# Kernel optimization log

Hardware: AMD Instinct MI355X
Metric: run time of the kernel (lower is better)

Reference implementation:

```python
import jax, jax.numpy as jnp
import numpy as np


def setup_inputs() -> dict:
    key = jax.random.key(0)
    k1, k2 = jax.random.split(key)
    z = jax.random.normal(k1, (16, 256, 32, 32), dtype=jnp.float32)
    emb = jax.random.normal(k2, (8192, 256), dtype=jnp.float32)
    return {"z": z, "emb": emb}


def reference(z, emb):
    B, C, H, W = z.shape
    # [B,C,H,W] -> [B*H*W, C], distances in fp32 for precision
    z_f = jnp.transpose(z, (0, 2, 3, 1)).reshape(-1, C).astype(jnp.float32)
    e = emb.astype(jnp.float32)
    # squared-distance expansion: ||z||^2 - 2 z.e + ||e||^2  -> [N, K]
    d = (
        jnp.sum(z_f * z_f, axis=1, keepdims=True)
        - 2.0 * (z_f @ e.T)
        + jnp.sum(e * e, axis=1)[None, :]
    )
    idx = jnp.argmin(d, axis=1)  # [N]
    out = emb[idx].astype(z.dtype)  # codebook gather
    return jnp.transpose(out.reshape(B, H, W, C), (0, 3, 1, 2))
```

## Files before the change

### kernel.cpp

```cpp
#include <hip/hip_runtime.h>
#include <stdint.h>

#define NB   16
#define CD   256
#define HW   1024
#define NQ   16384
#define KCN  8192

typedef unsigned long long u64;
typedef unsigned short     u16;
using f32x4  = __attribute__((ext_vector_type(4))) float;
using bf16x8 = __attribute__((ext_vector_type(8))) __bf16;

#define ZTB_OFF  0
#define EMBB_OFF 8388608
#define EH_OFF   12582912
#define CAND_OFF 12615680

static __device__ __forceinline__ void gl_lds16(const void* g, void* l) {
  __builtin_amdgcn_global_load_lds(
      (const __attribute__((address_space(1))) void*)g,
      (__attribute__((address_space(3))) void*)l, 16, 0, 0);
}

static __device__ __forceinline__ unsigned bf16r(float x) {
  unsigned u = __float_as_uint(x);
  return (u + 0x7fffu + ((u >> 16) & 1u)) >> 16;
}

static __device__ __forceinline__ u64 umin64(u64 a, u64 b) { return a < b ? a : b; }
static __device__ __forceinline__ u64 umax64(u64 a, u64 b) { return a < b ? b : a; }

__global__ __launch_bounds__(256) void k_prep(const float* __restrict__ z,
                                              const float* __restrict__ emb,
                                              u16* __restrict__ zTb,
                                              u16* __restrict__ embB,
                                              float* __restrict__ eH) {
  const int bx = (int)blockIdx.x;
  if (bx < 1024) {
    __shared__ float tile[64][65];
    const int b   = bx >> 6;
    const int hwT = (bx >> 2) & 15;
    const int cT  = bx & 3;
    const int tx  = threadIdx.x & 63;
    const int ty  = threadIdx.x >> 6;
    const float* src = z + (size_t)(b * CD + cT * 64) * HW + hwT * 64;
#pragma unroll
    for (int i = 0; i < 16; ++i) {
      const int c_l = ty + 4 * i;
      tile[c_l][tx] = src[(size_t)c_l * HW + tx];
    }
    __syncthreads();
    const size_t dbase = (size_t)(b * HW + hwT * 64) * CD + cT * 64;
#pragma unroll
    for (int i = 0; i < 16; ++i) {
      const int hw_l = ty + 4 * i;
      zTb[dbase + (size_t)hw_l * CD + tx] = (u16)bf16r(tile[tx][hw_l]);
    }
  } else {
    const int wave = (bx - 1024) * 4 + ((int)threadIdx.x >> 6);
    const int lane = threadIdx.x & 63;
#pragma unroll
    for (int it = 0; it < 8; ++it) {
      const int row = wave * 8 + it;
      const float4 v = *(const float4*)(emb + (size_t)row * CD + lane * 4);
      uint2 pk;
      pk.x = bf16r(v.x) | (bf16r(v.y) << 16);
      pk.y = bf16r(v.z) | (bf16r(v.w) << 16);
      *(uint2*)(embB + (size_t)row * CD + lane * 4) = pk;
      float s = v.x * v.x + v.y * v.y + v.z * v.z + v.w * v.w;
#pragma unroll
      for (int off = 32; off; off >>= 1) s += __shfl_xor(s, off, 64);
      if (lane == 0) eH[row] = 0.5f * s + 1024.0f;
    }
  }
}


#define WAITV(N) asm volatile("s_waitcnt vmcnt(" #N ")" ::: "memory")
#define MEMFENCE() asm volatile("" ::: "memory")

__global__ __launch_bounds__(256, 2) void k_argmin(const u16* __restrict__ zTb,
                                                   const u16* __restrict__ embB,
                                                   const float* __restrict__ eH,
                                                   u64* __restrict__ cand) {
  __shared__ __align__(16) u16 Bs[4][64 * 128];

  const int tid  = (int)threadIdx.x;
  const int w    = tid >> 6;
  const int lane = tid & 63;
  const int l15  = lane & 15, quad = lane >> 4;
  const int q0    = (int)(blockIdx.x >> 3) * 128;
  const int split = (int)(blockIdx.x & 7);
  const int wq0 = (w & 1) * 64;
  const int nh  = w >> 1;

  bf16x8 Af[4][2][4];
  {
    const char* aB = (const char*)zTb + (size_t)(q0 + wq0 + l15) * 512 + quad * 16;
#pragma unroll
    for (int i = 0; i < 4; ++i)
#pragma unroll
      for (int kc = 0; kc < 2; ++kc)
#pragma unroll
        for (int ks = 0; ks < 4; ++ks)
          Af[i][kc][ks] = *(const bf16x8*)(aB + i * 8192 + kc * 256 + ks * 64);
  }
  MEMFENCE();

  const char* bS = (const char*)embB + (size_t)split * 524288
                 + (size_t)(tid >> 4) * 512
                 + (size_t)(((tid & 15) ^ ((tid >> 4) & 7)) * 16);
  const int ldsW = tid * 16;

#define STAGE(RING, SRCOFF)                                                    \
  do {                                                                         \
    const char* _s = bP + (SRCOFF);                                            \
    char* _d = (char*)Bs[RING] + ldsW;                                         \
    gl_lds16(_s,         _d);                                                  \
    gl_lds16(_s + 8192,  _d + 4096);                                           \
    gl_lds16(_s + 16384, _d + 8192);                                           \
    gl_lds16(_s + 24576, _d + 12288);                                          \
    MEMFENCE();                                                                \
  } while (0)

  const int bRow = (nh * 32 + l15) * 256;
  const int gx   = l15 & 7;

#define MFMA_INT(RING, KCH)                                                    \
  do {                                                                         \
    const char* _b = (const char*)Bs[RING] + bRow;                             \
    __builtin_amdgcn_s_setprio(1);                                             \
    _Pragma("unroll")                                                          \
    for (int ks = 0; ks < 4; ++ks) {                                           \
      const int _o = ((ks * 4 + quad) ^ gx) * 16;                              \
      const bf16x8 bf0 = *(const bf16x8*)(_b + _o);                            \
      const bf16x8 bf1 = *(const bf16x8*)(_b + 4096 + _o);                     \
      _Pragma("unroll")                                                        \
      for (int i = 0; i < 4; ++i)                                              \
        acc[i][0] = __builtin_amdgcn_mfma_f32_16x16x32_bf16(Af[i][KCH][ks],    \
                                                            bf0, acc[i][0],    \
                                                            0, 0, 0);          \
      _Pragma("unroll")                                                        \
      for (int i = 0; i < 4; ++i)                                              \
        acc[i][1] = __builtin_amdgcn_mfma_f32_16x16x32_bf16(Af[i][KCH][ks],    \
                                                            bf1, acc[i][1],    \
                                                            0, 0, 0);          \
    }                                                                          \
    __builtin_amdgcn_s_setprio(0);                                             \
  } while (0)

#define ACCZERO()                                                              \
  do {                                                                         \
    _Pragma("unroll")                                                          \
    for (int i = 0; i < 4; ++i) {                                              \
      acc[i][0] = f32x4{0.f, 0.f, 0.f, 0.f};                                   \
      acc[i][1] = f32x4{0.f, 0.f, 0.f, 0.f};                                   \
    }                                                                          \
  } while (0)

#define EPILOGUE(NC, EH0, EH1)                                                 \
  do {                                                                         \
    _Pragma("unroll")                                                          \
    for (int i = 0; i < 4; ++i)                                                \
      _Pragma("unroll")                                                        \
      for (int r = 0; r < 4; ++r) {                                            \
        const int s = i * 4 + r;                                               \
        const unsigned kb0 = (__float_as_uint((EH0) - acc[i][0][r]) & ~31u)    \
                             | (unsigned)((NC) * 2 + 0);                       \
        const unsigned kb1 = (__float_as_uint((EH1) - acc[i][1][r]) & ~31u)    \
                             | (unsigned)((NC) * 2 + 1);                       \
        const float k0 = __uint_as_float(kb0), k1 = __uint_as_float(kb1);      \
        const float lo = fminf(k0, k1), hi = fmaxf(k0, k1);                    \
        b2[s] = fminf(fmaxf(lo, b1[s]), fminf(hi, b2[s]));                     \
        b1[s] = fminf(lo, b1[s]);                                              \
      }                                                                        \
  } while (0)

  f32x4 acc[4][2];
  float b1[16], b2[16];
  const float FMAX = __uint_as_float(0x7F7FFFFFu);
#pragma unroll
  for (int s = 0; s < 16; ++s) { b1[s] = FMAX; b2[s] = FMAX; }

  const float* ehP = eH + split * 1024 + nh * 32 + l15;
  float ehA[2], ehB[2], ehAn[2], ehBn[2];

  const char* bP = bS;
  STAGE(0, 0);
  ehA[0] = ehP[0];  ehA[1] = ehP[16];  MEMFENCE();
  STAGE(1, 256);
  STAGE(2, 32768);
  ehB[0] = ehP[64]; ehB[1] = ehP[80]; MEMFENCE();
  const float* ehPn = ehP + 128;

  for (int ntp = 0; ntp < 7; ++ntp) {
    const int nca = 2 * ntp, ncb = 2 * ntp + 1;

    ACCZERO();
    WAITV(12); __builtin_amdgcn_s_barrier(); MEMFENCE();
    STAGE(3, 33024);
    MFMA_INT(0, 0);

    WAITV(10); __builtin_amdgcn_s_barrier(); MEMFENCE();
    STAGE(0, 65536);
    ehAn[0] = ehPn[0]; ehAn[1] = ehPn[16]; MEMFENCE();
    MFMA_INT(1, 1);
    EPILOGUE(nca, ehA[0], ehA[1]);

    ACCZERO();
    WAITV(12); __builtin_amdgcn_s_barrier(); MEMFENCE();
    STAGE(1, 65792);
    MFMA_INT(2, 0);

    WAITV(10); __builtin_amdgcn_s_barrier(); MEMFENCE();
    STAGE(2, 98304);
    ehBn[0] = ehPn[64]; ehBn[1] = ehPn[80]; MEMFENCE();
    MFMA_INT(3, 1);
    EPILOGUE(ncb, ehB[0], ehB[1]);

    ehA[0] = ehAn[0]; ehA[1] = ehAn[1];
    ehB[0] = ehBn[0]; ehB[1] = ehBn[1];
    bP += 65536;
    ehPn += 128;
  }

  {
    ACCZERO();
    WAITV(12); __builtin_amdgcn_s_barrier(); MEMFENCE();
    STAGE(3, 33024);
    MFMA_INT(0, 0);

    WAITV(10); __builtin_amdgcn_s_barrier(); MEMFENCE();
    MFMA_INT(1, 1);
    EPILOGUE(14, ehA[0], ehA[1]);

    ACCZERO();
    WAITV(6); __builtin_amdgcn_s_barrier(); MEMFENCE();
    MFMA_INT(2, 0);

    WAITV(0); __builtin_amdgcn_s_barrier(); MEMFENCE();
    MFMA_INT(3, 1);
    EPILOGUE(15, ehB[0], ehB[1]);
  }
#undef STAGE
#undef MFMA_INT
#undef ACCZERO
#undef EPILOGUE

#pragma unroll
  for (int s = 0; s < 16; ++s) {
    u64 x1 = ((u64)__float_as_uint(b1[s]) << 32) | (unsigned)l15;
    u64 x2 = ((u64)__float_as_uint(b2[s]) << 32) | (unsigned)l15;
#pragma unroll
    for (int off = 1; off < 16; off <<= 1) {
      const u64 o1 = __shfl_xor(x1, off, 64);
      const u64 o2 = __shfl_xor(x2, off, 64);
      const u64 lo = umin64(x1, o1);
      const u64 hi = umax64(x1, o1);
      x1 = lo;
      x2 = umin64(hi, umin64(x2, o2));
    }
    if (l15 == 0) {
      const int i = s >> 2, r = s & 3;
      const int q = q0 + wq0 + i * 16 + quad * 4 + r;
      const unsigned kb1 = (unsigned)(x1 >> 32), kb2 = (unsigned)(x2 >> 32);
      const int id1 = (int)(kb1 & 31u), id2 = (int)(kb2 & 31u);
      const int n1 = split * 1024 + (id1 >> 1) * 64 + nh * 32
                     + (id1 & 1) * 16 + (int)(x1 & 15);
      const int n2 = split * 1024 + (id2 >> 1) * 64 + nh * 32
                     + (id2 & 1) * 16 + (int)(x2 & 15);
      cand[(size_t)q * 32 + split * 4 + nh * 2 + 0] = ((u64)kb1 << 32) | (unsigned)n1;
      cand[(size_t)q * 32 + split * 4 + nh * 2 + 1] = ((u64)kb2 << 32) | (unsigned)n2;
    }
  }
}

__global__ __launch_bounds__(256) void k_pick_out(const float* __restrict__ z,
                                                  const float* __restrict__ emb,
                                                  const u64* __restrict__ cand,
                                                  float* __restrict__ out) {
  __shared__ float zs[16][257];
  __shared__ float tile[16][257];
  const int t    = (int)threadIdx.x;
  const int lane = t & 63;
  const int wv   = t >> 6;
  const int sub  = lane >> 4;
  const int l15  = lane & 15;
  const int q0b  = (int)blockIdx.x * 16;
  const int b    = q0b >> 10, hw0 = q0b & 1023;
  const int q    = q0b + wv * 4 + sub;
  const int hwl  = wv * 4 + sub;

  {
    const float* zp = z + ((size_t)(b * CD + t)) * HW + hw0;
    const float4 a0 = *(const float4*)(zp + 0);
    const float4 a1 = *(const float4*)(zp + 4);
    const float4 a2 = *(const float4*)(zp + 8);
    const float4 a3 = *(const float4*)(zp + 12);
    zs[0][t] = a0.x;  zs[1][t] = a0.y;  zs[2][t] = a0.z;  zs[3][t] = a0.w;
    zs[4][t] = a1.x;  zs[5][t] = a1.y;  zs[6][t] = a1.z;  zs[7][t] = a1.w;
    zs[8][t] = a2.x;  zs[9][t] = a2.y;  zs[10][t] = a2.z; zs[11][t] = a2.w;
    zs[12][t] = a3.x; zs[13][t] = a3.y; zs[14][t] = a3.z; zs[15][t] = a3.w;
  }
  __syncthreads();

  const u64* cp = cand + (size_t)q * 32 + l15 * 2;
  const u64 v0 = cp[0], v1 = cp[1];
  u64 s0 = umin64(v0, v1), s1 = umax64(v0, v1), s2 = ~0ull, s3 = ~0ull;
#pragma unroll
  for (int off = 1; off < 16; off <<= 1) {
    const u64 b0 = __shfl_xor(s0, off, 64);
    const u64 b1 = __shfl_xor(s1, off, 64);
    const u64 b2 = __shfl_xor(s2, off, 64);
    const u64 b3 = __shfl_xor(s3, off, 64);
    const u64 c0 = umin64(s0, b0);
    const u64 c1 = umin64(umin64(s1, b1), umax64(s0, b0));
    const u64 c2 = umin64(umin64(s2, b2),
                          umin64(umax64(s1, b0), umax64(s0, b1)));
    const u64 c3 = umin64(umin64(umin64(s3, b3), umax64(s2, b0)),
                          umin64(umax64(s0, b2), umax64(s1, b1)));
    s0 = c0; s1 = c1; s2 = c2; s3 = c3;
  }
  const u64 sel[4] = {s0, s1, s2, s3};

  float zq[16];
#pragma unroll
  for (int j = 0; j < 16; ++j) zq[j] = zs[hwl][j * 16 + l15];

  double bd = 1e300;
  int bi = 0x7fffffff;
  float keep[16];
#pragma unroll
  for (int j = 0; j < 16; ++j) keep[j] = 0.f;
#pragma unroll
  for (int c4 = 0; c4 < 4; ++c4) {
    const int idx = (int)(unsigned)(sel[c4] & 0xffffffffull);
    const float* er = emb + (size_t)idx * CD;
    float ev[16];
#pragma unroll
    for (int j = 0; j < 16; ++j) ev[j] = er[j * 16 + l15];
    double s = 0.0;
#pragma unroll
    for (int j = 0; j < 16; ++j) {
      const double d = (double)zq[j] - (double)ev[j];
      s += d * d;
    }
#pragma unroll
    for (int off = 1; off < 16; off <<= 1) s += __shfl_xor(s, off, 64);
    const bool better = (s < bd) || (s == bd && idx < bi);
    if (better) {
      bd = s; bi = idx;
#pragma unroll
      for (int j = 0; j < 16; ++j) keep[j] = ev[j];
    }
  }
#pragma unroll
  for (int j = 0; j < 16; ++j) tile[hwl][j * 16 + l15] = keep[j];
  __syncthreads();
  const int cluster = t >> 4;
  const int ll      = t & 15;
  float* obase = out + (size_t)b * CD * HW + hw0 + ll;
#pragma unroll
  for (int j = 0; j < 16; ++j) {
    const int c = 16 * j + cluster;
    obase[(size_t)c * HW] = tile[ll][c];
  }
}

extern "C" void kernel_launch(void* const* d_in, const int* in_sizes, int n_in,
                              void* d_out, int out_size, void* d_ws, size_t ws_size,
                              hipStream_t stream) {
  const float* z   = (const float*)d_in[0];
  const float* emb = (const float*)d_in[1];
  float* out = (float*)d_out;

  char* ws = (char*)d_ws;
  u16*   zTb  = (u16*)(ws + ZTB_OFF);
  u16*   embB = (u16*)(ws + EMBB_OFF);
  float* eH   = (float*)(ws + EH_OFF);
  u64*   cand = (u64*)(ws + CAND_OFF);

  k_prep<<<1280, 256, 0, stream>>>(z, emb, zTb, embB, eH);
  k_argmin<<<1024, 256, 0, stream>>>(zTb, embB, eH, cand);
  k_pick_out<<<1024, 256, 0, stream>>>(z, emb, cand, out);
}
```

Before: 176.7 us.

## Give each wave a private LDS double buffer and drop block barriers

The 4-slot shared ring that all four waves filled cooperatively is replaced by a private two-slot LDS buffer per wave. Each wave stages only the codebook rows it consumes, so the s_barrier calls can go and waits use only vmcnt/lgkmcnt. All B fragments for a K-chunk are read from LDS up front, and the next chunk's global-to-LDS copy is issued into the same slot right after those reads. This removes block-wide synchronisation stalls between waves. The cost is that waves sharing the same rows now load them separately, so global traffic rises, and each wave has fewer tiles in flight.

```diff
diff --git a/kernel.cpp b/kernel.cpp
--- a/kernel.cpp
+++ b/kernel.cpp
@@ -78,13 +78,14 @@
 
 
 #define WAITV(N) asm volatile("s_waitcnt vmcnt(" #N ")" ::: "memory")
+#define LGKM0()  asm volatile("s_waitcnt lgkmcnt(0)" ::: "memory")
 #define MEMFENCE() asm volatile("" ::: "memory")
 
 __global__ __launch_bounds__(256, 2) void k_argmin(const u16* __restrict__ zTb,
                                                    const u16* __restrict__ embB,
                                                    const float* __restrict__ eH,
                                                    u64* __restrict__ cand) {
-  __shared__ __align__(16) u16 Bs[4][64 * 128];
+  __shared__ __align__(16) u16 Bs[4][2][4096];
 
   const int tid  = (int)threadIdx.x;
   const int w    = tid >> 6;
@@ -108,58 +109,94 @@
   }
   MEMFENCE();
 
-  const char* bS = (const char*)embB + (size_t)split * 524288
-                 + (size_t)(tid >> 4) * 512
-                 + (size_t)(((tid & 15) ^ ((tid >> 4) & 7)) * 16);
-  const int ldsW = tid * 16;
-
-#define STAGE(RING, SRCOFF)                                                    \
+  char* myLds0 = (char*)&Bs[w][0][0];
+  char* myLds1 = myLds0 + 8192;
+  const int lane16 = lane * 16;
+
+  const char* bW = (const char*)embB
+                 + (size_t)(split * 1024 + nh * 32 + (lane >> 3)) * 512
+                 + (size_t)(((lane & 7) ^ (lane >> 3)) * 16);
+
+#define STAGE(SLOT, SRC)                                                       \
   do {                                                                         \
-    const char* _s = bP + (SRCOFF);                                            \
-    char* _d = (char*)Bs[RING] + ldsW;                                         \
-    gl_lds16(_s,         _d);                                                  \
-    gl_lds16(_s + 8192,  _d + 4096);                                           \
-    gl_lds16(_s + 16384, _d + 8192);                                           \
-    gl_lds16(_s + 24576, _d + 12288);                                          \
+    const char* _s = (SRC);                                                    \
+    char* _d = (SLOT) + lane16;                                                \
+    gl_lds16(_s,          _d);                                                 \
+    gl_lds16(_s + 4096,   _d + 1024);                                          \
+    gl_lds16(_s + 8192,   _d + 2048);                                          \
+    gl_lds16(_s + 12288,  _d + 3072);                                          \
+    gl_lds16(_s + 128,    _d + 4096);                                          \
+    gl_lds16(_s + 4224,   _d + 5120);                                          \
+    gl_lds16(_s + 8320,   _d + 6144);                                          \
+    gl_lds16(_s + 12416,  _d + 7168);                                          \
     MEMFENCE();                                                                \
   } while (0)
 
-  const int bRow = (nh * 32 + l15) * 256;
-  const int gx   = l15 & 7;
-
-#define MFMA_INT(RING, KCH)                                                    \
+  const int gx = l15 & 7;
+  const int oA = (quad ^ gx) * 16;
+  const int oB = ((4 + quad) ^ gx) * 16;
+
+  f32x4 acc[4][2];
+  float b1[16], b2[16];
+  const float FMAX = __uint_as_float(0x7F7FFFFFu);
+#pragma unroll
+  for (int s = 0; s < 16; ++s) { b1[s] = FMAX; b2[s] = FMAX; }
+
+#define ACCZERO()                                                              \
   do {                                                                         \
-    const char* _b = (const char*)Bs[RING] + bRow;                             \
+    _Pragma("unroll")                                                          \
+    for (int i = 0; i < 4; ++i) {                                              \
+      acc[i][0] = f32x4{0.f, 0.f, 0.f, 0.f};                                   \
+      acc[i][1] = f32x4{0.f, 0.f, 0.f, 0.f};                                   \
+    }                                                                          \
+  } while (0)
+
+#define COMPUTE(SB, KC, ...)                                                   \
+  do {                                                                         \
+    const char* _sb = (const char*)(SB) + l15 * 128;                           \
+    bf16x8 f00 = *(const bf16x8*)(_sb + oA);                                   \
+    bf16x8 f01 = *(const bf16x8*)(_sb + 2048 + oA);                            \
+    bf16x8 f10 = *(const bf16x8*)(_sb + oB);                                   \
+    bf16x8 f11 = *(const bf16x8*)(_sb + 2048 + oB);                            \
+    bf16x8 f20 = *(const bf16x8*)(_sb + 4096 + oA);                            \
+    bf16x8 f21 = *(const bf16x8*)(_sb + 6144 + oA);                            \
+    bf16x8 f30 = *(const bf16x8*)(_sb + 4096 + oB);                            \
+    bf16x8 f31 = *(const bf16x8*)(_sb + 6144 + oB);                            \
+    LGKM0();                                                                   \
+    __VA_ARGS__;                                                               \
     __builtin_amdgcn_s_setprio(1);                                             \
     _Pragma("unroll")                                                          \
-    for (int ks = 0; ks < 4; ++ks) {                                           \
-      const int _o = ((ks * 4 + quad) ^ gx) * 16;                              \
-      const bf16x8 bf0 = *(const bf16x8*)(_b + _o);                            \
-      const bf16x8 bf1 = *(const bf16x8*)(_b + 4096 + _o);                     \
-      _Pragma("unroll")                                                        \
-      for (int i = 0; i < 4; ++i)                                              \
-        acc[i][0] = __builtin_amdgcn_mfma_f32_16x16x32_bf16(Af[i][KCH][ks],    \
-                                                            bf0, acc[i][0],    \
-                                                            0, 0, 0);          \
-      _Pragma("unroll")                                                        \
-      for (int i = 0; i < 4; ++i)                                              \
-        acc[i][1] = __builtin_amdgcn_mfma_f32_16x16x32_bf16(Af[i][KCH][ks],    \
-                                                            bf1, acc[i][1],    \
-                                                            0, 0, 0);          \
+    for (int i = 0; i < 4; ++i) {                                              \
+      acc[i][0] = __builtin_amdgcn_mfma_f32_16x16x32_bf16(Af[i][KC][0], f00,   \
+                                                          acc[i][0], 0, 0, 0); \
+      acc[i][1] = __builtin_amdgcn_mfma_f32_16x16x32_bf16(Af[i][KC][0], f01,   \
+                                                          acc[i][1], 0, 0, 0); \
+    }                                                                          \
+    _Pragma("unroll")                                                          \
+    for (int i = 0; i < 4; ++i) {                                              \
+      acc[i][0] = __builtin_amdgcn_mfma_f32_16x16x32_bf16(Af[i][KC][1], f10,   \
+                                                          acc[i][0], 0, 0, 0); \
+      acc[i][1] = __builtin_amdgcn_mfma_f32_16x16x32_bf16(Af[i][KC][1], f11,   \
+                                                          acc[i][1], 0, 0, 0); \
+    }                                                                          \
+    _Pragma("unroll")                                                          \
+    for (int i = 0; i < 4; ++i) {                                              \
+      acc[i][0] = __builtin_amdgcn_mfma_f32_16x16x32_bf16(Af[i][KC][2], f20,   \
+                                                          acc[i][0], 0, 0, 0); \
+      acc[i][1] = __builtin_amdgcn_mfma_f32_16x16x32_bf16(Af[i][KC][2], f21,   \
+                                                          acc[i][1], 0, 0, 0); \
+    }                                                                          \
+    _Pragma("unroll")                                                          \
+    for (int i = 0; i < 4; ++i) {                                              \
+      acc[i][0] = __builtin_amdgcn_mfma_f32_16x16x32_bf16(Af[i][KC][3], f30,   \
+                                                          acc[i][0], 0, 0, 0); \
+      acc[i][1] = __builtin_amdgcn_mfma_f32_16x16x32_bf16(Af[i][KC][3], f31,   \
+                                                          acc[i][1], 0, 0, 0); \
     }                                                                          \
     __builtin_amdgcn_s_setprio(0);                                             \
   } while (0)
 
-#define ACCZERO()                                                              \
-  do {                                                                         \
-    _Pragma("unroll")                                                          \
-    for (int i = 0; i < 4; ++i) {                                              \
-      acc[i][0] = f32x4{0.f, 0.f, 0.f, 0.f};                                   \
-      acc[i][1] = f32x4{0.f, 0.f, 0.f, 0.f};                                   \
-    }                                                                          \
-  } while (0)
-
-#define EPILOGUE(NC, EH0, EH1)                                                 \
+#define EPILOGUE(NT, EH0, EH1)                                                 \
   do {                                                                         \
     _Pragma("unroll")                                                          \
     for (int i = 0; i < 4; ++i)                                                \
@@ -167,9 +204,9 @@
       for (int r = 0; r < 4; ++r) {                                            \
         const int s = i * 4 + r;                                               \
         const unsigned kb0 = (__float_as_uint((EH0) - acc[i][0][r]) & ~31u)    \
-                             | (unsigned)((NC) * 2 + 0);                       \
+                             | (unsigned)((NT) * 2 + 0);                       \
         const unsigned kb1 = (__float_as_uint((EH1) - acc[i][1][r]) & ~31u)    \
-                             | (unsigned)((NC) * 2 + 1);                       \
+                             | (unsigned)((NT) * 2 + 1);                       \
         const float k0 = __uint_as_float(kb0), k1 = __uint_as_float(kb1);      \
         const float lo = fminf(k0, k1), hi = fmaxf(k0, k1);                    \
         b2[s] = fminf(fmaxf(lo, b1[s]), fminf(hi, b2[s]));                     \
@@ -177,74 +214,39 @@
       }                                                                        \
   } while (0)
 
-  f32x4 acc[4][2];
-  float b1[16], b2[16];
-  const float FMAX = __uint_as_float(0x7F7FFFFFu);
-#pragma unroll
-  for (int s = 0; s < 16; ++s) { b1[s] = FMAX; b2[s] = FMAX; }
-
   const float* ehP = eH + split * 1024 + nh * 32 + l15;
-  float ehA[2], ehB[2], ehAn[2], ehBn[2];
-
-  const char* bP = bS;
-  STAGE(0, 0);
-  ehA[0] = ehP[0];  ehA[1] = ehP[16];  MEMFENCE();
-  STAGE(1, 256);
-  STAGE(2, 32768);
-  ehB[0] = ehP[64]; ehB[1] = ehP[80]; MEMFENCE();
-  const float* ehPn = ehP + 128;
-
-  for (int ntp = 0; ntp < 7; ++ntp) {
-    const int nca = 2 * ntp, ncb = 2 * ntp + 1;
-
+  float ehA0, ehA1, ehN0 = 0.f, ehN1 = 0.f;
+
+  const char* bC = bW;
+  STAGE(myLds0, bC);
+  ehA0 = ehP[0]; ehA1 = ehP[16]; MEMFENCE();
+  STAGE(myLds1, bC + 256);
+  const float* ehN = ehP + 64;
+
+  for (int nt = 0; nt < 15; ++nt) {
     ACCZERO();
-    WAITV(12); __builtin_amdgcn_s_barrier(); MEMFENCE();
-    STAGE(3, 33024);
-    MFMA_INT(0, 0);
-
-    WAITV(10); __builtin_amdgcn_s_barrier(); MEMFENCE();
-    STAGE(0, 65536);
-    ehAn[0] = ehPn[0]; ehAn[1] = ehPn[16]; MEMFENCE();
-    MFMA_INT(1, 1);
-    EPILOGUE(nca, ehA[0], ehA[1]);
-
-    ACCZERO();
-    WAITV(12); __builtin_amdgcn_s_barrier(); MEMFENCE();
-    STAGE(1, 65792);
-    MFMA_INT(2, 0);
-
-    WAITV(10); __builtin_amdgcn_s_barrier(); MEMFENCE();
-    STAGE(2, 98304);
-    ehBn[0] = ehPn[64]; ehBn[1] = ehPn[80]; MEMFENCE();
-    MFMA_INT(3, 1);
-    EPILOGUE(ncb, ehB[0], ehB[1]);
-
-    ehA[0] = ehAn[0]; ehA[1] = ehAn[1];
-    ehB[0] = ehBn[0]; ehB[1] = ehBn[1];
-    bP += 65536;
-    ehPn += 128;
+    WAITV(10);
+    COMPUTE(myLds0, 0, STAGE(myLds0, bC + 32768));
+    WAITV(8);
+    COMPUTE(myLds1, 1,
+            { ehN0 = ehN[0]; ehN1 = ehN[16]; MEMFENCE();
+              STAGE(myLds1, bC + 32768 + 256); });
+    EPILOGUE(nt, ehA0, ehA1);
+    ehA0 = ehN0; ehA1 = ehN1;
+    bC += 32768;
+    ehN += 64;
   }
 
   {
     ACCZERO();
-    WAITV(12); __builtin_amdgcn_s_barrier(); MEMFENCE();
-    STAGE(3, 33024);
-    MFMA_INT(0, 0);
-
-    WAITV(10); __builtin_amdgcn_s_barrier(); MEMFENCE();
-    MFMA_INT(1, 1);
-    EPILOGUE(14, ehA[0], ehA[1]);
-
-    ACCZERO();
-    WAITV(6); __builtin_amdgcn_s_barrier(); MEMFENCE();
-    MFMA_INT(2, 0);
-
-    WAITV(0); __builtin_amdgcn_s_barrier(); MEMFENCE();
-    MFMA_INT(3, 1);
-    EPILOGUE(15, ehB[0], ehB[1]);
+    WAITV(10);
+    COMPUTE(myLds0, 0, {});
+    WAITV(0);
+    COMPUTE(myLds1, 1, {});
+    EPILOGUE(15, ehA0, ehA1);
   }
 #undef STAGE
-#undef MFMA_INT
+#undef COMPUTE
 #undef ACCZERO
 #undef EPILOGUE
 
```

New measurement: 179.3 us. About the same (+1.5%).
